# Kernel tuning notes

Hardware: AMD Instinct MI355X
Metric: run time of the kernel (lower is better)

The kernel has to match this reference:

```python
import jax, jax.numpy as jnp
import numpy as np

B, L, D = 2048, 200, 128
N_ITEMS = 100000


def _lin(k, fan_in, fan_out):
    s = 1.0 / np.sqrt(fan_in)
    kw, kb = jax.random.split(k)
    w = jax.random.uniform(kw, (fan_in, fan_out), jnp.float32, -s, s)
    b = jax.random.uniform(kb, (fan_out,), jnp.float32, -s, s)
    return w, b


def setup_inputs() -> dict:
    key = jax.random.key(0)
    ks = jax.random.split(key, 12)
    item_emb = jax.random.normal(ks[0], (N_ITEMS, D), jnp.float32).at[0].set(0.0)  # padding_idx=0
    item_bias_tab = jax.random.normal(ks[1], (N_ITEMS, 1), jnp.float32).at[0].set(0.0)
    aw1, ab1 = _lin(ks[2], 3 * D, 128)
    aw2, ab2 = _lin(ks[3], 128, 64)
    afw, afb = _lin(ks[4], 64, 1)
    nw, nb = _lin(ks[5], D, D)
    dw1, db1 = _lin(ks[6], 3 * D, 512)
    dw2, db2 = _lin(ks[7], 512, 256)
    dw3, db3 = _lin(ks[8], 256, 128)
    fw, fb = _lin(ks[9], 128, 1)
    in_item_id = jax.random.randint(ks[10], (B, L), 0, N_ITEMS, dtype=jnp.int32)
    item_id = jax.random.randint(ks[11], (B,), 0, N_ITEMS, dtype=jnp.int32)
    return dict(in_item_id=in_item_id, item_id=item_id, item_emb=item_emb,
                item_bias_tab=item_bias_tab, aw1=aw1, ab1=ab1, aw2=aw2, ab2=ab2,
                afw=afw, afb=afb, nw=nw, nb=nb, dw1=dw1, db1=db1, dw2=dw2, db2=db2,
                dw3=dw3, db3=db3, fw=fw, fb=fb)


def reference(in_item_id, item_id, item_emb, item_bias_tab,
              aw1, ab1, aw2, ab2, afw, afb, nw, nb,
              dw1, db1, dw2, db2, dw3, db3, fw, fb):
    sig = jax.nn.sigmoid
    seq_emb = item_emb[in_item_id]          # [B, L, D]
    target_emb = item_emb[item_id]          # [B, D]
    item_bias = item_bias_tab[item_id][:, 0]  # [B]

    t = target_emb[:, None, :]              # [B, 1, D] broadcast over L
    key = jnp.concatenate((jnp.broadcast_to(t, seq_emb.shape),
                           t * seq_emb,
                           t - seq_emb), axis=-1)  # [B, L, 3D]

    # feed-forward (DIN) attention scorer: MLP(key) -> scalar score per position
    h = sig(key @ aw1 + ab1)
    h = sig(h @ aw2 + ab2)
    score = (h @ afw + afb)[..., 0]         # [B, L]
    score = jnp.where(in_item_id == 0, 0.0, score)  # key_padding_mask, softmax=False
    attn_seq = jnp.einsum('bl,bld->bd', score, seq_emb)  # [B, D]

    attn_seq = attn_seq @ nw + nb           # norm Linear
    cat_emb = jnp.concatenate((attn_seq, target_emb, target_emb * attn_seq), axis=-1)  # [B, 3D]
    g = sig(cat_emb @ dw1 + db1)
    g = sig(g @ dw2 + db2)
    g = sig(g @ dw3 + db3)
    out = (g @ fw + fb)[:, 0]               # [B]
    return out + item_bias
```

## Files before the change

### kernel.cpp

```cpp
#include <hip/hip_runtime.h>
#include <hip/hip_bf16.h>
#include <stdint.h>

typedef __attribute__((ext_vector_type(8))) short bf8;
typedef __attribute__((ext_vector_type(4))) short bf4;
typedef __attribute__((ext_vector_type(4))) float f32x4;

#define MFMA16(a,b,c) __builtin_amdgcn_mfma_f32_16x16x32_bf16(a,b,c,0,0,0)

__device__ __forceinline__ unsigned short f2bf(float x){
  unsigned int u = __builtin_bit_cast(unsigned int, x);
  u = u + 0x7FFFu + ((u >> 16) & 1u);
  return (unsigned short)(u >> 16);
}
__device__ __forceinline__ unsigned short f2bfb(float x){
  __hip_bfloat16 h = __float2bfloat16(x);
  return __builtin_bit_cast(unsigned short, h);
}
__device__ __forceinline__ float bf2f(unsigned short h){
  unsigned int u = ((unsigned int)h) << 16;
  return __builtin_bit_cast(float, u);
}
__device__ __forceinline__ float sigm(float x){
  return __builtin_amdgcn_rcpf(1.0f + __expf(-x));
}
__device__ __forceinline__ int swzu(int row, int k, int Kd8){
  return (row*Kd8 + ((k>>3) ^ (row & 7)))*8 + (k & 7);
}

__global__ void k_prep(const float* __restrict__ aw1, const float* __restrict__ aw2,
                       const float* __restrict__ nw, const float* __restrict__ dw1,
                       const float* __restrict__ dw2, const float* __restrict__ dw3,
                       const float* __restrict__ emb,
                       unsigned short* __restrict__ WbT, unsigned short* __restrict__ WcT,
                       unsigned short* __restrict__ Wsum, unsigned short* __restrict__ A2T,
                       unsigned short* __restrict__ NWT, unsigned short* __restrict__ D1T,
                       unsigned short* __restrict__ D2T, unsigned short* __restrict__ D3T,
                       unsigned short* __restrict__ EMBB)
{
  int n = blockIdx.x*256 + threadIdx.x;
  int stride = gridDim.x*256;
  for (int i = n; i < 1600000; i += stride){
    const float4* s = (const float4*)(emb + (size_t)i*8);
    float4 a = s[0], b = s[1];
    bf8 o;
    o[0]=(short)f2bf(a.x); o[1]=(short)f2bf(a.y); o[2]=(short)f2bf(a.z); o[3]=(short)f2bf(a.w);
    o[4]=(short)f2bf(b.x); o[5]=(short)f2bf(b.y); o[6]=(short)f2bf(b.z); o[7]=(short)f2bf(b.w);
    ((bf8*)EMBB)[i] = o;
  }
  for (int i = n; i < 16384; i += stride){
    int j = i >> 7, k = i & 127;
    WbT[i] = f2bf(aw1[(128+k)*128 + j]);
    WcT[i] = f2bf(aw1[(256+k)*128 + j]);
  }
  for (int i = n; i < 16384; i += stride){
    int j = i >> 7, k = i & 127;
    Wsum[i] = f2bf(aw1[k*128 + j] + aw1[(256+k)*128 + j]);
  }
  for (int i = n; i < 8192; i += stride){
    int j = i >> 7, k = i & 127;
    A2T[i] = f2bf(aw2[k*64 + j]);
  }
  for (int i = n; i < 16384; i += stride){
    int j = i >> 7, k = i & 127;
    NWT[i] = f2bf(nw[k*128 + j]);
  }
  for (int i = n; i < 196608; i += stride){
    int j = i / 384, k = i - j*384;
    D1T[i] = f2bf(dw1[k*512 + j]);
  }
  for (int i = n; i < 131072; i += stride){
    int j = i >> 9, k = i & 511;
    D2T[i] = f2bf(dw2[k*256 + j]);
  }
  for (int i = n; i < 32768; i += stride){
    int j = i >> 8, k = i & 255;
    D3T[i] = f2bf(dw3[k*128 + j]);
  }
}

__global__ __launch_bounds__(256, 4) void k_attn(
    const int* __restrict__ in_ids, const int* __restrict__ item_id,
    const float* __restrict__ emb, const unsigned short* __restrict__ embb,
    const float* __restrict__ ab1, const float* __restrict__ ab2v,
    const float* __restrict__ afw, const float* __restrict__ afb,
    const unsigned short* __restrict__ WbT, const unsigned short* __restrict__ WcT,
    const unsigned short* __restrict__ Wsum, const unsigned short* __restrict__ A2T,
    float* __restrict__ attn_raw)
{
  __shared__ __align__(16) unsigned short sS[32*128];
  __shared__ __align__(16) unsigned short sH[32*128];
  __shared__ float sT[128];
  __shared__ float sC0[128];
  __shared__ float sP2[2][128];
  __shared__ float sPart[4][32];
  __shared__ int   sIds[32];

  const int b = blockIdx.x;
  const int tid = threadIdx.x;
  const int wave = tid >> 6, lane = tid & 63;
  const int lr = lane & 15, lg = lane >> 4;

  const int tgt = item_id[b];
  if (tid < 128) sT[tid] = emb[(size_t)tgt*128 + tid];
  __syncthreads();

  {
    int j = tid & 127, hf = tid >> 7;
    const unsigned short* wsrow = Wsum + j*128 + hf*64;
    float p = 0.f;
    #pragma unroll
    for (int c = 0; c < 8; ++c){
      bf8 wv = *(const bf8*)(wsrow + c*8);
      #pragma unroll
      for (int e = 0; e < 8; ++e)
        p += sT[hf*64 + c*8 + e] * bf2f((unsigned short)wv[e]);
    }
    sP2[hf][j] = p;
  }
  __syncthreads();
  if (tid < 128) sC0[tid] = ab1[tid] + sP2[0][tid] + sP2[1][tid];

  bf8 wfrag[2][4];
  {
    const float4* sT4 = (const float4*)sT;
    #pragma unroll
    for (int mt = 0; mt < 2; ++mt){
      int j = (wave + mt*4)*16 + lr;
      #pragma unroll
      for (int kk = 0; kk < 4; ++kk){
        bf8 wb = *(const bf8*)(WbT + j*128 + kk*32 + lg*8);
        bf8 wc = *(const bf8*)(WcT + j*128 + kk*32 + lg*8);
        float4 t0 = sT4[kk*8 + lg*2];
        float4 t1 = sT4[kk*8 + lg*2 + 1];
        float tv[8] = {t0.x,t0.y,t0.z,t0.w,t1.x,t1.y,t1.z,t1.w};
        bf8 o;
        #pragma unroll
        for (int e = 0; e < 8; ++e)
          o[e] = (short)f2bfb(tv[e]*bf2f((unsigned short)wb[e]) - bf2f((unsigned short)wc[e]));
        wfrag[mt][kk] = o;
      }
    }
  }
  bf8 a2frag[4];
  #pragma unroll
  for (int kk = 0; kk < 4; ++kk)
    a2frag[kk] = *(const bf8*)(A2T + (wave*16+lr)*128 + kk*32 + lg*8);

  float b2r[4], afr[4];
  #pragma unroll
  for (int i = 0; i < 4; ++i){
    int j2 = wave*16 + lg*4 + i;
    b2r[i] = ab2v[j2];
    afr[i] = afw[j2];
  }
  const float afbv = afb[0];
  __syncthreads();
  float c0r[2][4];
  #pragma unroll
  for (int mt = 0; mt < 2; ++mt)
    #pragma unroll
    for (int i = 0; i < 4; ++i)
      c0r[mt][i] = sC0[(wave + mt*4)*16 + lg*4 + i];

  float facc8[8] = {0,0,0,0,0,0,0,0};
  const bf8* S8 = (const bf8*)sS;
  const bf8* H8 = (const bf8*)sH;
  const int rg = tid >> 4, cg = tid & 15;
  const int sxm = lr & 7;
  const int chv = tid & 15;
  const int rowq = tid >> 4;

  bf8 stg0, stg1; int id0, id1;
  {
    id0 = in_ids[b*200 + rowq];
    stg0 = *(const bf8*)(embb + (size_t)id0*128 + chv*8);
    id1 = in_ids[b*200 + 16 + rowq];
    stg1 = *(const bf8*)(embb + (size_t)id1*128 + chv*8);
  }

  for (int rt = 0; rt < 7; ++rt){
    __syncthreads();
    if (chv == 0){ sIds[rowq] = id0; sIds[16 + rowq] = id1; }
    ((bf8*)sS)[rowq*16 + (chv ^ (rowq & 7))] = stg0;
    {
      int r2 = 16 + rowq;
      ((bf8*)sS)[r2*16 + (chv ^ (r2 & 7))] = stg1;
    }
    if (rt < 6){
      int l0 = (rt+1)*32 + rowq;
      id0 = (l0 < 200) ? in_ids[b*200 + l0] : 0;
      stg0 = *(const bf8*)(embb + (size_t)id0*128 + chv*8);
      int l1 = l0 + 16;
      id1 = (l1 < 200) ? in_ids[b*200 + l1] : 0;
      stg1 = *(const bf8*)(embb + (size_t)id1*128 + chv*8);
    }
    __syncthreads();
    f32x4 acc1[2][2] = {};
    #pragma unroll
    for (int kk = 0; kk < 4; ++kk){
      int kx = (kk*4 + lg) ^ sxm;
      bf8 s0 = S8[lr*16 + kx];
      bf8 s1 = S8[(16+lr)*16 + kx];
      acc1[0][0] = MFMA16(wfrag[0][kk], s0, acc1[0][0]);
      acc1[0][1] = MFMA16(wfrag[0][kk], s1, acc1[0][1]);
      acc1[1][0] = MFMA16(wfrag[1][kk], s0, acc1[1][0]);
      acc1[1][1] = MFMA16(wfrag[1][kk], s1, acc1[1][1]);
    }
    #pragma unroll
    for (int mt = 0; mt < 2; ++mt)
      #pragma unroll
      for (int nt = 0; nt < 2; ++nt){
        int r = nt*16 + lr;
        int j0 = (wave + mt*4)*16 + lg*4;
        bf4 q4;
        #pragma unroll
        for (int i = 0; i < 4; ++i)
          q4[i] = (short)f2bfb(sigm(acc1[mt][nt][i] + c0r[mt][i]));
        int idx = (r*16 + ((j0 >> 3) ^ (r & 7)))*8 + (j0 & 7);
        *(bf4*)(sH + idx) = q4;
      }
    __syncthreads();
    f32x4 acc2[2] = {};
    #pragma unroll
    for (int kk = 0; kk < 4; ++kk){
      int kx = (kk*4 + lg) ^ sxm;
      bf8 h0 = H8[lr*16 + kx];
      bf8 h1f = H8[(16+lr)*16 + kx];
      acc2[0] = MFMA16(a2frag[kk], h0, acc2[0]);
      acc2[1] = MFMA16(a2frag[kk], h1f, acc2[1]);
    }
    float part0 = 0.f, part1 = 0.f;
    #pragma unroll
    for (int i = 0; i < 4; ++i){
      part0 += sigm(acc2[0][i] + b2r[i]) * afr[i];
      part1 += sigm(acc2[1][i] + b2r[i]) * afr[i];
    }
    part0 += __shfl_xor(part0, 16); part0 += __shfl_xor(part0, 32);
    part1 += __shfl_xor(part1, 16); part1 += __shfl_xor(part1, 32);
    if (lg == 0){ sPart[wave][lr] = part0; sPart[wave][16+lr] = part1; }
    __syncthreads();
    #pragma unroll
    for (int q = 0; q < 2; ++q){
      int r = rg*2 + q;
      int l = rt*32 + r;
      float sc = sPart[0][r] + sPart[1][r] + sPart[2][r] + sPart[3][r] + afbv;
      sc = (l < 200 && sIds[r] != 0) ? sc : 0.f;
      bf8 v = S8[r*16 + (cg ^ (r & 7))];
      #pragma unroll
      for (int e = 0; e < 8; ++e)
        facc8[e] += sc * bf2f((unsigned short)v[e]);
    }
  }
  __syncthreads();
  float* red = (float*)sS;
  #pragma unroll
  for (int e = 0; e < 8; ++e) red[tid*8 + e] = facc8[e];
  __syncthreads();
  if (tid < 128){
    float s = 0.f;
    #pragma unroll
    for (int g = 0; g < 16; ++g) s += red[g*128 + tid];
    attn_raw[(size_t)b*128 + tid] = s;
  }
}

__global__ __launch_bounds__(512) void k_deep(
    const int* __restrict__ item_id, const float* __restrict__ emb,
    const float* __restrict__ bias_tab,
    const float* __restrict__ nbv,
    const float* __restrict__ db1, const float* __restrict__ db2,
    const float* __restrict__ db3, const float* __restrict__ fw,
    const float* __restrict__ fb,
    const unsigned short* __restrict__ NWT, const unsigned short* __restrict__ D1T,
    const unsigned short* __restrict__ D2T, const unsigned short* __restrict__ D3T,
    const float* __restrict__ attn_raw, float* __restrict__ out)
{
  __shared__ __align__(16) unsigned short sA[16*128];
  __shared__ float sTf[16*128];
  __shared__ __align__(16) unsigned short sCat[16*384];
  __shared__ __align__(16) unsigned short sG1[16*512];
  __shared__ __align__(16) unsigned short sG2[16*256];
  __shared__ __align__(16) unsigned short sG3[16*128];
  __shared__ float sNB[128], sDB1[512], sDB2[256], sDB3[128], sFWd[128];
  __shared__ float sBias[16];

  const int r0 = blockIdx.x * 16;
  const int tid = threadIdx.x;
  const int wave = tid >> 6, lane = tid & 63;
  const int lr = lane & 15, lg = lane >> 4;
  const int sx = lr & 7;

  if (tid < 128){ sNB[tid] = nbv[tid]; sDB3[tid] = db3[tid]; sFWd[tid] = fw[tid]; }
  sDB1[tid] = db1[tid];
  if (tid < 256) sDB2[tid] = db2[tid];
  if (tid < 16) sBias[tid] = bias_tab[item_id[r0 + tid]];

  if (tid < 256){
    int r = tid >> 4, ch = tid & 15;
    const float* asrc = attn_raw + (size_t)(r0 + r)*128 + ch*8;
    float4 v0 = *(const float4*)asrc;
    float4 v1 = *(const float4*)(asrc + 4);
    bf8 o;
    o[0]=(short)f2bf(v0.x); o[1]=(short)f2bf(v0.y); o[2]=(short)f2bf(v0.z); o[3]=(short)f2bf(v0.w);
    o[4]=(short)f2bf(v1.x); o[5]=(short)f2bf(v1.y); o[6]=(short)f2bf(v1.z); o[7]=(short)f2bf(v1.w);
    ((bf8*)sA)[r*16 + (ch ^ (r & 7))] = o;
    int id = item_id[r0 + r];
    const float* tsrc = emb + (size_t)id*128 + ch*8;
    float4 t0 = *(const float4*)tsrc;
    float4 t1 = *(const float4*)(tsrc + 4);
    *(float4*)(sTf + r*128 + ch*8)     = t0;
    *(float4*)(sTf + r*128 + ch*8 + 4) = t1;
  }
  __syncthreads();

  {
    const bf8* A8 = (const bf8*)sA;
    int ct = wave;
    f32x4 acc = {};
    #pragma unroll
    for (int kk = 0; kk < 4; ++kk){
      int kx = (kk*4 + lg) ^ sx;
      bf8 af = A8[lr*16 + kx];
      bf8 bw = *(const bf8*)(NWT + (ct*16+lr)*128 + kk*32 + lg*8);
      acc = MFMA16(af, bw, acc);
    }
    int col = ct*16 + lr;
    float nbc = sNB[col];
    #pragma unroll
    for (int i = 0; i < 4; ++i){
      int r = lg*4 + i;
      float x = acc[i] + nbc;
      float tv = sTf[r*128 + col];
      sCat[swzu(r, col,      48)] = f2bf(x);
      sCat[swzu(r, 128+col,  48)] = f2bf(tv);
      sCat[swzu(r, 256+col,  48)] = f2bf(tv * x);
    }
  }
  __syncthreads();
  {
    const bf8* C8 = (const bf8*)sCat;
    #pragma unroll
    for (int c = 0; c < 4; ++c){
      int ct = wave + c*8;
      f32x4 acc = {};
      #pragma unroll
      for (int kk = 0; kk < 12; ++kk){
        int kx = (kk*4 + lg) ^ sx;
        bf8 af = C8[lr*48 + kx];
        bf8 bw = *(const bf8*)(D1T + (size_t)(ct*16+lr)*384 + kk*32 + lg*8);
        acc = MFMA16(af, bw, acc);
      }
      int col = ct*16 + lr;
      float bb = sDB1[col];
      #pragma unroll
      for (int i = 0; i < 4; ++i)
        sG1[swzu(lg*4 + i, col, 64)] = f2bf(sigm(acc[i] + bb));
    }
  }
  __syncthreads();
  {
    const bf8* G8 = (const bf8*)sG1;
    #pragma unroll
    for (int c = 0; c < 2; ++c){
      int ct = wave + c*8;
      f32x4 acc = {};
      #pragma unroll
      for (int kk = 0; kk < 16; ++kk){
        int kx = (kk*4 + lg) ^ sx;
        bf8 af = G8[lr*64 + kx];
        bf8 bw = *(const bf8*)(D2T + (size_t)(ct*16+lr)*512 + kk*32 + lg*8);
        acc = MFMA16(af, bw, acc);
      }
      int col = ct*16 + lr;
      float bb = sDB2[col];
      #pragma unroll
      for (int i = 0; i < 4; ++i)
        sG2[swzu(lg*4 + i, col, 32)] = f2bf(sigm(acc[i] + bb));
    }
  }
  __syncthreads();
  {
    const bf8* G8 = (const bf8*)sG2;
    int ct = wave;
    f32x4 acc = {};
    #pragma unroll
    for (int kk = 0; kk < 8; ++kk){
      int kx = (kk*4 + lg) ^ sx;
      bf8 af = G8[lr*32 + kx];
      bf8 bw = *(const bf8*)(D3T + (size_t)(ct*16+lr)*256 + kk*32 + lg*8);
      acc = MFMA16(af, bw, acc);
    }
    int col = ct*16 + lr;
    float bb = sDB3[col];
    #pragma unroll
    for (int i = 0; i < 4; ++i)
      sG3[swzu(lg*4 + i, col, 16)] = f2bf(sigm(acc[i] + bb));
  }
  __syncthreads();
  if (tid < 128){
    int r = tid >> 3, seg = tid & 7;
    float p = 0.f;
    #pragma unroll
    for (int c = 0; c < 16; ++c)
      p += bf2f(sG3[swzu(r, seg*16 + c, 16)]) * sFWd[seg*16 + c];
    p += __shfl_xor(p, 1);
    p += __shfl_xor(p, 2);
    p += __shfl_xor(p, 4);
    if (seg == 0) out[r0 + r] = p + fb[0] + sBias[r];
  }
}

extern "C" void kernel_launch(void* const* d_in, const int* in_sizes, int n_in,
                              void* d_out, int out_size, void* d_ws, size_t ws_size,
                              hipStream_t stream) {
  const int*   in_ids   = (const int*)d_in[0];
  const int*   item_id  = (const int*)d_in[1];
  const float* emb      = (const float*)d_in[2];
  const float* bias_tab = (const float*)d_in[3];
  const float* aw1 = (const float*)d_in[4];
  const float* ab1 = (const float*)d_in[5];
  const float* aw2 = (const float*)d_in[6];
  const float* ab2 = (const float*)d_in[7];
  const float* afw = (const float*)d_in[8];
  const float* afb = (const float*)d_in[9];
  const float* nw  = (const float*)d_in[10];
  const float* nb  = (const float*)d_in[11];
  const float* dw1 = (const float*)d_in[12];
  const float* db1 = (const float*)d_in[13];
  const float* dw2 = (const float*)d_in[14];
  const float* db2 = (const float*)d_in[15];
  const float* dw3 = (const float*)d_in[16];
  const float* db3 = (const float*)d_in[17];
  const float* fw  = (const float*)d_in[18];
  const float* fb  = (const float*)d_in[19];
  float* outp = (float*)d_out;

  char* ws = (char*)d_ws;
  float* attn_raw = (float*)ws;
  unsigned short* WbT  = (unsigned short*)(ws + 1048576);
  unsigned short* WcT  = WbT  + 16384;
  unsigned short* Wsum = WcT  + 16384;
  unsigned short* A2T  = Wsum + 16384;
  unsigned short* NWT  = A2T  + 8192;
  unsigned short* D1T  = NWT  + 16384;
  unsigned short* D2T  = D1T  + 196608;
  unsigned short* D3T  = D2T  + 131072;
  unsigned short* EMBB = D3T  + 32768;

  hipLaunchKernelGGL(k_prep, dim3(2048), dim3(256), 0, stream,
                     aw1, aw2, nw, dw1, dw2, dw3, emb,
                     WbT, WcT, Wsum, A2T, NWT, D1T, D2T, D3T, EMBB);
  hipLaunchKernelGGL(k_attn, dim3(2048), dim3(256), 0, stream,
                     in_ids, item_id, emb, EMBB, ab1, ab2, afw, afb,
                     WbT, WcT, Wsum, A2T, attn_raw);
  hipLaunchKernelGGL(k_deep, dim3(128), dim3(512), 0, stream,
                     item_id, emb, bias_tab, nb, db1, db2, db3, fw, fb,
                     NWT, D1T, D2T, D3T, attn_raw, outp);
}
```

Before: 118.3 us.

## Split attention sequence across two blocks per batch row with double-buffered tiles

Each batch row's 7 sequence tiles are now split over two blocks (4 and 3 tiles), doubling the grid. The partial sums are written to separate buffers and added in k_deep. The embedding tile buffer is double-buffered, which drops one barrier per iteration, and the first gather is issued before the target-embedding setup so its latency is hidden. The cost is that each block repeats the per-row weight-fragment setup, and shared memory grows, which may lower occupancy.

New measurement: 162.3 us. 1.37x slower.

```diff
diff --git a/kernel.cpp b/kernel.cpp
--- a/kernel.cpp
+++ b/kernel.cpp
@@ -86,20 +86,34 @@
     const float* __restrict__ afw, const float* __restrict__ afb,
     const unsigned short* __restrict__ WbT, const unsigned short* __restrict__ WcT,
     const unsigned short* __restrict__ Wsum, const unsigned short* __restrict__ A2T,
-    float* __restrict__ attn_raw)
+    float* __restrict__ attn_part)
 {
-  __shared__ __align__(16) unsigned short sS[32*128];
+  __shared__ __align__(16) unsigned short sS[2][32*128];
   __shared__ __align__(16) unsigned short sH[32*128];
   __shared__ float sT[128];
   __shared__ float sC0[128];
   __shared__ float sP2[2][128];
-  __shared__ float sPart[4][32];
-  __shared__ int   sIds[32];
-
-  const int b = blockIdx.x;
+  __shared__ __align__(16) float sPart[32][4];
+  __shared__ int   sIds[2][32];
+
+  const int bid = blockIdx.x;
+  const int b = bid >> 1, h = bid & 1;
+  const int t0 = h * 4;
+  const int nt = 4 - h;
   const int tid = threadIdx.x;
   const int wave = tid >> 6, lane = tid & 63;
   const int lr = lane & 15, lg = lane >> 4;
+  const int rowq = tid >> 4, chv = tid & 15;
+
+  bf8 stg0, stg1; int id0, id1;
+  {
+    int l0 = t0*32 + rowq;
+    id0 = in_ids[b*200 + l0];
+    stg0 = *(const bf8*)(embb + (size_t)id0*128 + chv*8);
+    int l1 = l0 + 16;
+    id1 = in_ids[b*200 + l1];
+    stg1 = *(const bf8*)(embb + (size_t)id1*128 + chv*8);
+  }
 
   const int tgt = item_id[b];
   if (tid < 128) sT[tid] = emb[(size_t)tgt*128 + tid];
@@ -131,9 +145,9 @@
       for (int kk = 0; kk < 4; ++kk){
         bf8 wb = *(const bf8*)(WbT + j*128 + kk*32 + lg*8);
         bf8 wc = *(const bf8*)(WcT + j*128 + kk*32 + lg*8);
-        float4 t0 = sT4[kk*8 + lg*2];
-        float4 t1 = sT4[kk*8 + lg*2 + 1];
-        float tv[8] = {t0.x,t0.y,t0.z,t0.w,t1.x,t1.y,t1.z,t1.w};
+        float4 q0 = sT4[kk*8 + lg*2];
+        float4 q1 = sT4[kk*8 + lg*2 + 1];
+        float tv[8] = {q0.x,q0.y,q0.z,q0.w,q1.x,q1.y,q1.z,q1.w};
         bf8 o;
         #pragma unroll
         for (int e = 0; e < 8; ++e)
@@ -164,31 +178,21 @@
       c0r[mt][i] = sC0[(wave + mt*4)*16 + lg*4 + i];
 
   float facc8[8] = {0,0,0,0,0,0,0,0};
-  const bf8* S8 = (const bf8*)sS;
   const bf8* H8 = (const bf8*)sH;
-  const int rg = tid >> 4, cg = tid & 15;
   const int sxm = lr & 7;
-  const int chv = tid & 15;
-  const int rowq = tid >> 4;
-
-  bf8 stg0, stg1; int id0, id1;
-  {
-    id0 = in_ids[b*200 + rowq];
-    stg0 = *(const bf8*)(embb + (size_t)id0*128 + chv*8);
-    id1 = in_ids[b*200 + 16 + rowq];
-    stg1 = *(const bf8*)(embb + (size_t)id1*128 + chv*8);
-  }
-
-  for (int rt = 0; rt < 7; ++rt){
-    __syncthreads();
-    if (chv == 0){ sIds[rowq] = id0; sIds[16 + rowq] = id1; }
-    ((bf8*)sS)[rowq*16 + (chv ^ (rowq & 7))] = stg0;
+
+  for (int it = 0; it < nt; ++it){
+    const int cb = it & 1;
+    unsigned short* sSc = sS[cb];
+    const bf8* S8 = (const bf8*)sSc;
+    if (chv == 0){ sIds[cb][rowq] = id0; sIds[cb][16+rowq] = id1; }
+    ((bf8*)sSc)[rowq*16 + (chv ^ (rowq & 7))] = stg0;
     {
       int r2 = 16 + rowq;
-      ((bf8*)sS)[r2*16 + (chv ^ (r2 & 7))] = stg1;
-    }
-    if (rt < 6){
-      int l0 = (rt+1)*32 + rowq;
+      ((bf8*)sSc)[r2*16 + (chv ^ (r2 & 7))] = stg1;
+    }
+    if (it + 1 < nt){
+      int l0 = (t0 + it + 1)*32 + rowq;
       id0 = (l0 < 200) ? in_ids[b*200 + l0] : 0;
       stg0 = *(const bf8*)(embb + (size_t)id0*128 + chv*8);
       int l1 = l0 + 16;
@@ -210,13 +214,13 @@
     #pragma unroll
     for (int mt = 0; mt < 2; ++mt)
       #pragma unroll
-      for (int nt = 0; nt < 2; ++nt){
-        int r = nt*16 + lr;
+      for (int ntl = 0; ntl < 2; ++ntl){
+        int r = ntl*16 + lr;
         int j0 = (wave + mt*4)*16 + lg*4;
         bf4 q4;
         #pragma unroll
         for (int i = 0; i < 4; ++i)
-          q4[i] = (short)f2bfb(sigm(acc1[mt][nt][i] + c0r[mt][i]));
+          q4[i] = (short)f2bfb(sigm(acc1[mt][ntl][i] + c0r[mt][i]));
         int idx = (r*16 + ((j0 >> 3) ^ (r & 7)))*8 + (j0 & 7);
         *(bf4*)(sH + idx) = q4;
       }
@@ -238,15 +242,16 @@
     }
     part0 += __shfl_xor(part0, 16); part0 += __shfl_xor(part0, 32);
     part1 += __shfl_xor(part1, 16); part1 += __shfl_xor(part1, 32);
-    if (lg == 0){ sPart[wave][lr] = part0; sPart[wave][16+lr] = part1; }
+    if (lg == 0){ sPart[lr][wave] = part0; sPart[16+lr][wave] = part1; }
     __syncthreads();
     #pragma unroll
     for (int q = 0; q < 2; ++q){
-      int r = rg*2 + q;
-      int l = rt*32 + r;
-      float sc = sPart[0][r] + sPart[1][r] + sPart[2][r] + sPart[3][r] + afbv;
-      sc = (l < 200 && sIds[r] != 0) ? sc : 0.f;
-      bf8 v = S8[r*16 + (cg ^ (r & 7))];
+      int r = rowq*2 + q;
+      int l = (t0 + it)*32 + r;
+      float4 pv = *(const float4*)&sPart[r][0];
+      float sc = pv.x + pv.y + pv.z + pv.w + afbv;
+      sc = (l < 200 && sIds[cb][r] != 0) ? sc : 0.f;
+      bf8 v = S8[r*16 + (chv ^ (r & 7))];
       #pragma unroll
       for (int e = 0; e < 8; ++e)
         facc8[e] += sc * bf2f((unsigned short)v[e]);
@@ -261,7 +266,7 @@
     float s = 0.f;
     #pragma unroll
     for (int g = 0; g < 16; ++g) s += red[g*128 + tid];
-    attn_raw[(size_t)b*128 + tid] = s;
+    attn_part[((size_t)h*2048 + b)*128 + tid] = s;
   }
 }
 
@@ -274,7 +279,7 @@
     const float* __restrict__ fb,
     const unsigned short* __restrict__ NWT, const unsigned short* __restrict__ D1T,
     const unsigned short* __restrict__ D2T, const unsigned short* __restrict__ D3T,
-    const float* __restrict__ attn_raw, float* __restrict__ out)
+    const float* __restrict__ attn_part, float* __restrict__ out)
 {
   __shared__ __align__(16) unsigned short sA[16*128];
   __shared__ float sTf[16*128];
@@ -298,9 +303,14 @@
 
   if (tid < 256){
     int r = tid >> 4, ch = tid & 15;
-    const float* asrc = attn_raw + (size_t)(r0 + r)*128 + ch*8;
-    float4 v0 = *(const float4*)asrc;
-    float4 v1 = *(const float4*)(asrc + 4);
+    const float* a0 = attn_part + (size_t)(r0 + r)*128 + ch*8;
+    const float* a1 = a0 + (size_t)2048*128;
+    float4 v0 = *(const float4*)a0;
+    float4 v1 = *(const float4*)(a0 + 4);
+    float4 w0 = *(const float4*)a1;
+    float4 w1 = *(const float4*)(a1 + 4);
+    v0.x+=w0.x; v0.y+=w0.y; v0.z+=w0.z; v0.w+=w0.w;
+    v1.x+=w1.x; v1.y+=w1.y; v1.z+=w1.z; v1.w+=w1.w;
     bf8 o;
     o[0]=(short)f2bf(v0.x); o[1]=(short)f2bf(v0.y); o[2]=(short)f2bf(v0.z); o[3]=(short)f2bf(v0.w);
     o[4]=(short)f2bf(v1.x); o[5]=(short)f2bf(v1.y); o[6]=(short)f2bf(v1.z); o[7]=(short)f2bf(v1.w);
@@ -437,8 +447,8 @@
   float* outp = (float*)d_out;
 
   char* ws = (char*)d_ws;
-  float* attn_raw = (float*)ws;
-  unsigned short* WbT  = (unsigned short*)(ws + 1048576);
+  float* attn_part = (float*)ws;
+  unsigned short* WbT  = (unsigned short*)(ws + 2097152);
   unsigned short* WcT  = WbT  + 16384;
   unsigned short* Wsum = WcT  + 16384;
   unsigned short* A2T  = Wsum + 16384;
@@ -451,10 +461,10 @@
   hipLaunchKernelGGL(k_prep, dim3(2048), dim3(256), 0, stream,
                      aw1, aw2, nw, dw1, dw2, dw3, emb,
                      WbT, WcT, Wsum, A2T, NWT, D1T, D2T, D3T, EMBB);
-  hipLaunchKernelGGL(k_attn, dim3(2048), dim3(256), 0, stream,
+  hipLaunchKernelGGL(k_attn, dim3(4096), dim3(256), 0, stream,
                      in_ids, item_id, emb, EMBB, ab1, ab2, afw, afb,
-                     WbT, WcT, Wsum, A2T, attn_raw);
+                     WbT, WcT, Wsum, A2T, attn_part);
   hipLaunchKernelGGL(k_deep, dim3(128), dim3(512), 0, stream,
                      item_id, emb, bias_tab, nb, db1, db2, db3, fw, fb,
-                     NWT, D1T, D2T, D3T, attn_raw, outp);
-}
+                     NWT, D1T, D2T, D3T, attn_part, outp);
+}
```
